# Kernel optimization log

Hardware: AMD Instinct MI355X
Metric: run time of the kernel (lower is better)

The kernel has to match this reference:

```python
import jax, jax.numpy as jnp
import numpy as np

SEQ_LEN, BATCH, N_IN, N_OUT, EMB, OUT_LEN = 256, 2048, 64, 64, 128, 128


def _uniform(key, shape, k):
    return jax.random.uniform(key, shape, jnp.float32, -k, k)


def setup_inputs() -> dict:
    key = jax.random.key(0)
    ks = jax.random.split(key, 9)
    kH = 1.0 / np.sqrt(EMB)
    return {
        "x": jax.random.normal(ks[0], (SEQ_LEN, BATCH, N_IN), jnp.float32),
        # encoder LSTM (input_size=N_IN, hidden=EMB), torch gate order i,f,g,o
        "enc_Wih": _uniform(ks[1], (4 * EMB, N_IN), kH),
        "enc_Whh": _uniform(ks[2], (4 * EMB, EMB), kH),
        "enc_b": _uniform(ks[3], (4 * EMB,), kH),
        # decoder LSTM (input_size=N_OUT, hidden=EMB)
        "dec_Wih": _uniform(ks[4], (4 * EMB, N_OUT), kH),
        "dec_Whh": _uniform(ks[5], (4 * EMB, EMB), kH),
        "dec_b": _uniform(ks[6], (4 * EMB,), kH),
        # output Linear EMB -> N_OUT
        "out_W": _uniform(ks[7], (N_OUT, EMB), kH),
        "out_b": _uniform(ks[8], (N_OUT,), kH),
    }


def _lstm_cell(h, c, xt, Wih, Whh, b):
    # torch gate order: i, f, g, o
    gates = xt @ Wih.T + h @ Whh.T + b  # [B, 4H]
    i, f, g, o = jnp.split(gates, 4, axis=-1)
    i, f, o = jax.nn.sigmoid(i), jax.nn.sigmoid(f), jax.nn.sigmoid(o)
    g = jnp.tanh(g)
    c_new = f * c + i * g
    h_new = o * jnp.tanh(c_new)
    return h_new, c_new


def reference(x, enc_Wih, enc_Whh, enc_b, dec_Wih, dec_Whh, dec_b, out_W, out_b):
    B = x.shape[1]
    h0 = jnp.zeros((B, EMB), x.dtype)
    c0 = jnp.zeros((B, EMB), x.dtype)

    # ---- encoder: scan over seq_len ----
    def enc_step(carry, xt):
        h, c = carry
        h, c = _lstm_cell(h, c, xt, enc_Wih, enc_Whh, enc_b)
        return (h, c), None

    (h, c), _ = jax.lax.scan(enc_step, (h0, c0), x)

    x0 = jnp.zeros((B, N_OUT), x.dtype)

    def dec_step(carry, _):
        xt, h, c = carry
        h, c = _lstm_cell(h, c, xt, dec_Wih, dec_Whh, dec_b)
        y = h @ out_W.T + out_b  # [B, N_OUT]
        return (y, h, c), y

    _, ys = jax.lax.scan(dec_step, (x0, h, c), None, length=OUT_LEN)  # [T, B, N_OUT]
    return jnp.transpose(ys, (1, 2, 0))  # [B, N_OUT, T]
```

## Files before the change

### kernel.cpp

```cpp
#include <hip/hip_runtime.h>

#define SEQ    256
#define BATCHN 2048
#define NIN    64
#define H      128
#define NOUT   64
#define TOUT   128
#define BT     16
#define ASTR   200
#define TCH    16
#define WSTR   136

using half8 = _Float16 __attribute__((ext_vector_type(8)));
using f32x4 = float    __attribute__((ext_vector_type(4)));

__device__ __forceinline__ float sigf(float v) {
    return __builtin_amdgcn_rcpf(1.f + __expf(-v));
}
__device__ __forceinline__ float tanhfast(float v) {
    return 1.f - 2.f * __builtin_amdgcn_rcpf(1.f + __expf(2.f * v));
}

__device__ __forceinline__ half8 ldfrag8(const float* __restrict__ p) {
    half8 r;
#pragma unroll
    for (int e = 0; e < 8; ++e) r[e] = (_Float16)p[e];
    return r;
}

__global__ __launch_bounds__(512, 2) void seq2seq_fused(
    const float* __restrict__ x,
    const float* __restrict__ eWih, const float* __restrict__ eWhh, const float* __restrict__ eb,
    const float* __restrict__ dWih, const float* __restrict__ dWhh, const float* __restrict__ db,
    const float* __restrict__ oW,   const float* __restrict__ obv,
    float* __restrict__ out)
{
    __shared__ __align__(16) _Float16 als[2][BT][ASTR];
    __shared__ __align__(16) _Float16 ybuf[TCH][BT][68];

    const int tid  = threadIdx.x;
    const int lane = tid & 63;
    const int w    = tid >> 6;
    const int jl   = lane & 15;
    const int lg   = lane >> 4;
    const int b0   = blockIdx.x * BT;

    float c[4] = {0.f, 0.f, 0.f, 0.f};

    half8 wf[4][6];
    float bq[4];
#pragma unroll
    for (int q = 0; q < 4; ++q) {
        const int j = q * H + w * 16 + jl;
#pragma unroll
        for (int kc = 0; kc < 2; ++kc)
            wf[q][kc] = ldfrag8(eWih + j * NIN + kc * 32 + lg * 8);
#pragma unroll
        for (int kc = 2; kc < 6; ++kc)
            wf[q][kc] = ldfrag8(eWhh + j * H + (kc - 2) * 32 + lg * 8);
        bq[q] = eb[j];
    }

    for (int i = tid; i < 2 * BT * ASTR; i += 512) ((_Float16*)als)[i] = (_Float16)0.f;
    __syncthreads();
    const int xi = tid >> 5, xn = (tid & 31) * 2;
    {
        const float2 xv = *(const float2*)(x + (b0 + xi) * NIN + xn);
        als[0][xi][xn]     = (_Float16)xv.x;
        als[0][xi][xn + 1] = (_Float16)xv.y;
    }
    __syncthreads();

    for (int t = 0; t < SEQ; ++t) {
        const int cur = t & 1, nxt = cur ^ 1;

        float2 xv = make_float2(0.f, 0.f);
        if (t + 1 < SEQ)
            xv = *(const float2*)(x + ((size_t)(t + 1) * BATCHN + b0 + xi) * NIN + xn);

        half8 af[6];
#pragma unroll
        for (int kc = 0; kc < 6; ++kc)
            af[kc] = *(const half8*)&als[cur][jl][kc * 32 + lg * 8];

        f32x4 ac[4];
#pragma unroll
        for (int q = 0; q < 4; ++q) {
            f32x4 a = {bq[q], bq[q], bq[q], bq[q]};
#pragma unroll
            for (int kc = 0; kc < 6; ++kc)
                a = __builtin_amdgcn_mfma_f32_16x16x32_f16(af[kc], wf[q][kc], a, 0, 0, 0);
            ac[q] = a;
        }

#pragma unroll
        for (int r = 0; r < 4; ++r) {
            const float ig = sigf(ac[0][r]);
            const float fg = sigf(ac[1][r]);
            const float gg = tanhfast(ac[2][r]);
            const float og = sigf(ac[3][r]);
            c[r] = fg * c[r] + ig * gg;
            const float hv = og * tanhfast(c[r]);
            als[nxt][lg * 4 + r][NIN + w * 16 + jl] = (_Float16)hv;
        }
        als[nxt][xi][xn]     = (_Float16)xv.x;
        als[nxt][xi][xn + 1] = (_Float16)xv.y;
        __syncthreads();
    }

#pragma unroll
    for (int q = 0; q < 4; ++q) {
        const int j = q * H + w * 16 + jl;
#pragma unroll
        for (int kc = 0; kc < 4; ++kc)
            wf[q][kc] = ldfrag8(dWhh + j * H + kc * 32 + lg * 8);
        bq[q] = db[j];
    }
    {
        half8 af[4];
#pragma unroll
        for (int kc = 0; kc < 4; ++kc)
            af[kc] = *(const half8*)&als[0][jl][NIN + kc * 32 + lg * 8];
        f32x4 ac[4];
#pragma unroll
        for (int q = 0; q < 4; ++q) {
            f32x4 a = {bq[q], bq[q], bq[q], bq[q]};
#pragma unroll
            for (int kc = 0; kc < 4; ++kc)
                a = __builtin_amdgcn_mfma_f32_16x16x32_f16(af[kc], wf[q][kc], a, 0, 0, 0);
            ac[q] = a;
        }
#pragma unroll
        for (int r = 0; r < 4; ++r) {
            const float ig = sigf(ac[0][r]);
            const float fg = sigf(ac[1][r]);
            const float gg = tanhfast(ac[2][r]);
            const float og = sigf(ac[3][r]);
            c[r] = fg * c[r] + ig * gg;
            const float hv = og * tanhfast(c[r]);
            als[1][lg * 4 + r][NIN + w * 16 + jl] = (_Float16)hv;
        }
        __syncthreads();
    }

    half8 of[4];
    float oB = 0.f;
    if (w < 4) {
        const int j = w * 16 + jl;
#pragma unroll
        for (int kc = 0; kc < 4; ++kc)
            of[kc] = ldfrag8(oW + j * H + kc * 32 + lg * 8);
        oB = obv[j];
    }

    {
        _Float16* mybuf = ((_Float16*)ybuf) + (size_t)w * 16 * WSTR;
#pragma unroll
        for (int q = 0; q < 4; ++q) {
            const int jb = q * H + w * 16;
            half8 afp[2];
#pragma unroll
            for (int k2 = 0; k2 < 2; ++k2)
                afp[k2] = ldfrag8(dWih + (jb + jl) * NIN + k2 * 32 + lg * 8);
#pragma unroll 1
            for (int nt = 0; nt < 8; ++nt) {
                half8 bf0, bf1;
#pragma unroll
                for (int e = 0; e < 8; ++e) {
                    bf0[e] = (_Float16)oW[(lg * 8 + e) * H + nt * 16 + jl];
                    bf1[e] = (_Float16)oW[(32 + lg * 8 + e) * H + nt * 16 + jl];
                }
                f32x4 acc;
#pragma unroll
                for (int r = 0; r < 4; ++r)
                    acc[r] = dWhh[(jb + lg * 4 + r) * H + nt * 16 + jl];
                acc = __builtin_amdgcn_mfma_f32_16x16x32_f16(afp[0], bf0, acc, 0, 0, 0);
                acc = __builtin_amdgcn_mfma_f32_16x16x32_f16(afp[1], bf1, acc, 0, 0, 0);
#pragma unroll
                for (int r = 0; r < 4; ++r)
                    mybuf[(lg * 4 + r) * WSTR + nt * 16 + jl] = (_Float16)acc[r];
            }
            __syncthreads();
#pragma unroll
            for (int kc = 0; kc < 4; ++kc)
                wf[q][kc] = *(const half8*)&mybuf[jl * WSTR + kc * 32 + lg * 8];
            float s = db[jb + jl];
            for (int m = 0; m < NIN; ++m) s += dWih[(jb + jl) * NIN + m] * obv[m];
            bq[q] = s;
            __syncthreads();
        }
    }

    for (int i = 1; i <= TOUT; ++i) {
        const int cur = i & 1, nxt = cur ^ 1;

        half8 af[4];
#pragma unroll
        for (int kc = 0; kc < 4; ++kc)
            af[kc] = *(const half8*)&als[cur][jl][NIN + kc * 32 + lg * 8];

        if (w < 4) {
            f32x4 ya = {oB, oB, oB, oB};
#pragma unroll
            for (int kc = 0; kc < 4; ++kc)
                ya = __builtin_amdgcn_mfma_f32_16x16x32_f16(af[kc], of[kc], ya, 0, 0, 0);
            const int tt = (i - 1) & (TCH - 1);
            const int j = w * 16 + jl;
#pragma unroll
            for (int r = 0; r < 4; ++r)
                ybuf[tt][lg * 4 + r][j] = (_Float16)ya[r];
        }

        if (i < TOUT) {
            f32x4 ac[4];
#pragma unroll
            for (int q = 0; q < 4; ++q) {
                f32x4 a = {bq[q], bq[q], bq[q], bq[q]};
#pragma unroll
                for (int kc = 0; kc < 4; ++kc)
                    a = __builtin_amdgcn_mfma_f32_16x16x32_f16(af[kc], wf[q][kc], a, 0, 0, 0);
                ac[q] = a;
            }
#pragma unroll
            for (int r = 0; r < 4; ++r) {
                const float ig = sigf(ac[0][r]);
                const float fg = sigf(ac[1][r]);
                const float gg = tanhfast(ac[2][r]);
                const float og = sigf(ac[3][r]);
                c[r] = fg * c[r] + ig * gg;
                const float hv = og * tanhfast(c[r]);
                als[nxt][lg * 4 + r][NIN + w * 16 + jl] = (_Float16)hv;
            }
        }
        __syncthreads();

        if ((i & (TCH - 1)) == 0) {
            const int t0 = i - TCH;
#pragma unroll
            for (int it = 0; it < 8; ++it) {
                const int slot = it * 512 + tid;
                const int pair = slot >> 2;
                const int tq   = slot & 3;
                const int row  = pair >> 6;
                const int j    = pair & 63;
                float4 v;
                v.x = (float)ybuf[tq * 4 + 0][row][j];
                v.y = (float)ybuf[tq * 4 + 1][row][j];
                v.z = (float)ybuf[tq * 4 + 2][row][j];
                v.w = (float)ybuf[tq * 4 + 3][row][j];
                *(float4*)(out + ((size_t)(b0 + row) * NOUT + j) * TOUT + t0 + tq * 4) = v;
            }
            __syncthreads();
        }
    }
}

extern "C" void kernel_launch(void* const* d_in, const int* in_sizes, int n_in,
                              void* d_out, int out_size, void* d_ws, size_t ws_size,
                              hipStream_t stream) {
    (void)in_sizes; (void)n_in; (void)out_size; (void)d_ws; (void)ws_size;
    const float* x    = (const float*)d_in[0];
    const float* eWih = (const float*)d_in[1];
    const float* eWhh = (const float*)d_in[2];
    const float* eb   = (const float*)d_in[3];
    const float* dWih = (const float*)d_in[4];
    const float* dWhh = (const float*)d_in[5];
    const float* db   = (const float*)d_in[6];
    const float* oW   = (const float*)d_in[7];
    const float* ob   = (const float*)d_in[8];

    seq2seq_fused<<<BATCHN / BT, 512, 0, stream>>>(
        x, eWih, eWhh, eb, dWih, dWhh, db, oW, ob, (float*)d_out);
}
```

Measured before the change: 453.3 us.

## Precompute folded decoder weights in separate kernel and split encoder/decoder

Moves the per-block computation of the folded decoder recurrence weight (Whh + Wih·oW) and bias into a one-time prep kernel writing fp16 results to workspace. Splits the fused kernel into encoder and decoder kernels that pass h and c through global workspace. This removes redundant per-block weight folding (128 blocks each redoing it) at the cost of two extra launches and a global round trip for the hidden state.

```diff
diff --git a/kernel.cpp b/kernel.cpp
--- a/kernel.cpp
+++ b/kernel.cpp
@@ -9,18 +9,17 @@
 #define BT     16
 #define ASTR   200
 #define TCH    16
-#define WSTR   136
 
 using half8 = _Float16 __attribute__((ext_vector_type(8)));
 using f32x4 = float    __attribute__((ext_vector_type(4)));
 
+
 __device__ __forceinline__ float sigf(float v) {
     return __builtin_amdgcn_rcpf(1.f + __expf(-v));
 }
 __device__ __forceinline__ float tanhfast(float v) {
     return 1.f - 2.f * __builtin_amdgcn_rcpf(1.f + __expf(2.f * v));
 }
-
 __device__ __forceinline__ half8 ldfrag8(const float* __restrict__ p) {
     half8 r;
 #pragma unroll
@@ -28,15 +27,35 @@
     return r;
 }
 
-__global__ __launch_bounds__(512, 2) void seq2seq_fused(
+__global__ __launch_bounds__(512) void prep_wp(
+    const float* __restrict__ dWih, const float* __restrict__ dWhh, const float* __restrict__ db,
+    const float* __restrict__ oW,   const float* __restrict__ obv,
+    _Float16* __restrict__ Wp, float* __restrict__ bp)
+{
+    const int b = blockIdx.x;
+    if (b < 128) {
+        const int idx = b * 512 + (int)threadIdx.x;
+        const int j = idx >> 7, n = idx & 127;
+        float s = dWhh[j * H + n];
+        const float* wr = dWih + j * NIN;
+#pragma unroll 8
+        for (int m = 0; m < NIN; ++m) s += wr[m] * oW[m * H + n];
+        Wp[idx] = (_Float16)s;
+    } else {
+        const int j = (int)threadIdx.x;
+        float s = db[j];
+        const float* wr = dWih + j * NIN;
+        for (int m = 0; m < NIN; ++m) s += wr[m] * obv[m];
+        bp[j] = s;
+    }
+}
+
+__global__ __launch_bounds__(512, 2) void enc_kernel(
     const float* __restrict__ x,
     const float* __restrict__ eWih, const float* __restrict__ eWhh, const float* __restrict__ eb,
-    const float* __restrict__ dWih, const float* __restrict__ dWhh, const float* __restrict__ db,
-    const float* __restrict__ oW,   const float* __restrict__ obv,
-    float* __restrict__ out)
+    _Float16* __restrict__ hws, float* __restrict__ cws)
 {
     __shared__ __align__(16) _Float16 als[2][BT][ASTR];
-    __shared__ __align__(16) _Float16 ybuf[TCH][BT][68];
 
     const int tid  = threadIdx.x;
     const int lane = tid & 63;
@@ -45,8 +64,6 @@
     const int lg   = lane >> 4;
     const int b0   = blockIdx.x * BT;
 
-    float c[4] = {0.f, 0.f, 0.f, 0.f};
-
     half8 wf[4][6];
     float bq[4];
 #pragma unroll
@@ -60,6 +77,8 @@
             wf[q][kc] = ldfrag8(eWhh + j * H + (kc - 2) * 32 + lg * 8);
         bq[q] = eb[j];
     }
+
+    float c[4] = {0.f, 0.f, 0.f, 0.f};
 
     for (int i = tid; i < 2 * BT * ASTR; i += 512) ((_Float16*)als)[i] = (_Float16)0.f;
     __syncthreads();
@@ -107,7 +126,47 @@
         als[nxt][xi][xn + 1] = (_Float16)xv.y;
         __syncthreads();
     }
-
+#pragma unroll
+    for (int k = 0; k < 4; ++k) {
+        const int idx = tid + k * 512;
+        const int row = idx >> 7, n = idx & 127;
+        hws[(size_t)(b0 + row) * H + n] = als[0][row][NIN + n];
+    }
+#pragma unroll
+    for (int r = 0; r < 4; ++r)
+        cws[(size_t)(b0 + lg * 4 + r) * H + w * 16 + jl] = c[r];
+}
+
+__global__ __launch_bounds__(512, 2) void dec_kernel(
+    const float* __restrict__ dWhh, const float* __restrict__ db,
+    const float* __restrict__ oW,   const float* __restrict__ obv,
+    const _Float16* __restrict__ Wp, const float* __restrict__ bp,
+    const _Float16* __restrict__ hws, const float* __restrict__ cws,
+    float* __restrict__ out)
+{
+    __shared__ __align__(16) _Float16 als[2][BT][ASTR];
+    __shared__ __align__(16) _Float16 ybuf[TCH][BT][68];
+
+    const int tid  = threadIdx.x;
+    const int lane = tid & 63;
+    const int w    = tid >> 6;
+    const int jl   = lane & 15;
+    const int lg   = lane >> 4;
+    const int b0   = blockIdx.x * BT;
+
+#pragma unroll
+    for (int k = 0; k < 4; ++k) {
+        const int idx = tid + k * 512;
+        const int row = idx >> 7, n = idx & 127;
+        als[0][row][NIN + n] = hws[(size_t)(b0 + row) * H + n];
+    }
+    float c[4];
+#pragma unroll
+    for (int r = 0; r < 4; ++r)
+        c[r] = cws[(size_t)(b0 + lg * 4 + r) * H + w * 16 + jl];
+
+    half8 wf[4][4];
+    float bq[4];
 #pragma unroll
     for (int q = 0; q < 4; ++q) {
         const int j = q * H + w * 16 + jl;
@@ -116,6 +175,17 @@
             wf[q][kc] = ldfrag8(dWhh + j * H + kc * 32 + lg * 8);
         bq[q] = db[j];
     }
+    half8 of[4];
+    float oB = 0.f;
+    if (w < 4) {
+        const int j = w * 16 + jl;
+#pragma unroll
+        for (int kc = 0; kc < 4; ++kc)
+            of[kc] = ldfrag8(oW + j * H + kc * 32 + lg * 8);
+        oB = obv[j];
+    }
+    __syncthreads();
+
     {
         half8 af[4];
 #pragma unroll
@@ -140,56 +210,17 @@
             const float hv = og * tanhfast(c[r]);
             als[1][lg * 4 + r][NIN + w * 16 + jl] = (_Float16)hv;
         }
-        __syncthreads();
-    }
-
-    half8 of[4];
-    float oB = 0.f;
-    if (w < 4) {
-        const int j = w * 16 + jl;
-#pragma unroll
-        for (int kc = 0; kc < 4; ++kc)
-            of[kc] = ldfrag8(oW + j * H + kc * 32 + lg * 8);
-        oB = obv[j];
-    }
-
-    {
-        _Float16* mybuf = ((_Float16*)ybuf) + (size_t)w * 16 * WSTR;
-#pragma unroll
-        for (int q = 0; q < 4; ++q) {
-            const int jb = q * H + w * 16;
-            half8 afp[2];
-#pragma unroll
-            for (int k2 = 0; k2 < 2; ++k2)
-                afp[k2] = ldfrag8(dWih + (jb + jl) * NIN + k2 * 32 + lg * 8);
-#pragma unroll 1
-            for (int nt = 0; nt < 8; ++nt) {
-                half8 bf0, bf1;
-#pragma unroll
-                for (int e = 0; e < 8; ++e) {
-                    bf0[e] = (_Float16)oW[(lg * 8 + e) * H + nt * 16 + jl];
-                    bf1[e] = (_Float16)oW[(32 + lg * 8 + e) * H + nt * 16 + jl];
-                }
-                f32x4 acc;
-#pragma unroll
-                for (int r = 0; r < 4; ++r)
-                    acc[r] = dWhh[(jb + lg * 4 + r) * H + nt * 16 + jl];
-                acc = __builtin_amdgcn_mfma_f32_16x16x32_f16(afp[0], bf0, acc, 0, 0, 0);
-                acc = __builtin_amdgcn_mfma_f32_16x16x32_f16(afp[1], bf1, acc, 0, 0, 0);
-#pragma unroll
-                for (int r = 0; r < 4; ++r)
-                    mybuf[(lg * 4 + r) * WSTR + nt * 16 + jl] = (_Float16)acc[r];
-            }
-            __syncthreads();
-#pragma unroll
-            for (int kc = 0; kc < 4; ++kc)
-                wf[q][kc] = *(const half8*)&mybuf[jl * WSTR + kc * 32 + lg * 8];
-            float s = db[jb + jl];
-            for (int m = 0; m < NIN; ++m) s += dWih[(jb + jl) * NIN + m] * obv[m];
-            bq[q] = s;
-            __syncthreads();
-        }
-    }
+    }
+
+#pragma unroll
+    for (int q = 0; q < 4; ++q) {
+        const int j = q * H + w * 16 + jl;
+#pragma unroll
+        for (int kc = 0; kc < 4; ++kc)
+            wf[q][kc] = *(const half8*)&Wp[(size_t)j * H + kc * 32 + lg * 8];
+        bq[q] = bp[j];
+    }
+    __syncthreads();
 
     for (int i = 1; i <= TOUT; ++i) {
         const int cur = i & 1, nxt = cur ^ 1;
@@ -258,7 +289,7 @@
 extern "C" void kernel_launch(void* const* d_in, const int* in_sizes, int n_in,
                               void* d_out, int out_size, void* d_ws, size_t ws_size,
                               hipStream_t stream) {
-    (void)in_sizes; (void)n_in; (void)out_size; (void)d_ws; (void)ws_size;
+    (void)in_sizes; (void)n_in; (void)out_size; (void)ws_size;
     const float* x    = (const float*)d_in[0];
     const float* eWih = (const float*)d_in[1];
     const float* eWhh = (const float*)d_in[2];
@@ -269,6 +300,14 @@
     const float* oW   = (const float*)d_in[7];
     const float* ob   = (const float*)d_in[8];
 
-    seq2seq_fused<<<BATCHN / BT, 512, 0, stream>>>(
-        x, eWih, eWhh, eb, dWih, dWhh, db, oW, ob, (float*)d_out);
-}
+    char* ws = (char*)d_ws;
+    _Float16* Wp  = (_Float16*)(ws);
+    float*    bp  = (float*)(ws + 131072);
+    _Float16* hws = (_Float16*)(ws + 262144);
+    float*    cws = (float*)(ws + 786432);
+
+    prep_wp   <<<129, 512, 0, stream>>>(dWih, dWhh, db, oW, ob, Wp, bp);
+    enc_kernel<<<BATCHN / BT, 512, 0, stream>>>(x, eWih, eWhh, eb, hws, cws);
+    dec_kernel<<<BATCHN / BT, 512, 0, stream>>>(dWhh, db, oW, ob, Wp, bp, hws, cws,
+                                                (float*)d_out);
+}
```

New measurement: 436.5 us. -3.7%, faster.
